# Kernel optimization log

Hardware: AMD Instinct MI355X
Metric: run time of the kernel (lower is better)

The kernel has to match this reference:

```python
import jax, jax.numpy as jnp
import numpy as np

N = 4096
IN_DIM = 256
OUT_DIM = 256
E = 131072


def setup_inputs() -> dict:
    key = jax.random.key(0)
    ks = jax.random.split(key, 8)
    x = jax.random.normal(ks[0], (N, IN_DIM), dtype=jnp.float32)
    edge_index = jax.random.randint(ks[1], (2, E), 0, N, dtype=jnp.int64)
    lap = jax.random.normal(ks[2], (N, N), dtype=jnp.float32)
    d_inv = jax.random.normal(ks[3], (N, N), dtype=jnp.float32)
    # parameters
    W_high = jax.random.normal(ks[4], (IN_DIM, OUT_DIM), dtype=jnp.float32) / np.sqrt(IN_DIM)
    W_conv = jax.random.normal(ks[5], (IN_DIM, OUT_DIM), dtype=jnp.float32) / np.sqrt(IN_DIM)
    b_conv = jnp.zeros((OUT_DIM,), dtype=jnp.float32)
    aL = jax.random.uniform(ks[6], (1,), dtype=jnp.float32)
    aH = jax.random.uniform(ks[7], (1,), dtype=jnp.float32)
    return {"x": x, "edge_index": edge_index, "lap": lap, "d_inv": d_inv,
            "W_high": W_high, "W_conv": W_conv, "b_conv": b_conv,
            "aL": aL, "aH": aH}


def _gcn_conv(x, edge_index, W, b, num_nodes):
    # PyG GCNConv: add self-loops, symmetric normalization, aggregate at target.
    src, dst = edge_index[0], edge_index[1]
    loop = jnp.arange(num_nodes, dtype=edge_index.dtype)
    src_f = jnp.concatenate([src, loop])
    dst_f = jnp.concatenate([dst, loop])
    deg = jax.ops.segment_sum(jnp.ones_like(dst_f, dtype=x.dtype), dst_f,
                              num_segments=num_nodes)
    deg_inv_sqrt = jnp.where(deg > 0, jax.lax.rsqrt(jnp.maximum(deg, 1e-12)), 0.0)
    norm = deg_inv_sqrt[src_f] * deg_inv_sqrt[dst_f]  # [E+N]
    xw = x @ W                                        # [N, out]
    msgs = xw[src_f] * norm[:, None]                  # [E+N, out]
    out = jax.ops.segment_sum(msgs, dst_f, num_segments=num_nodes)
    return out + b


def reference(x, edge_index, lap, d_inv, W_high, W_conv, b_conv, aL, aH):
    # high-pass branch: Lhp = d_inv @ lap @ d_inv; Hh = Lhp @ relu(x @ W_high)
    Lhp = (d_inv @ lap) @ d_inv
    Hh = Lhp @ jax.nn.relu(x @ W_high)
    # low-pass branch: GCNConv
    Hl = _gcn_conv(x, edge_index, W_conv, b_conv, x.shape[0])
    return aL * Hl + aH * Hh
```

## Files before the change

### kernel.cpp

```cpp
#include <hip/hip_runtime.h>

#define NN 4096
#define DD 256
#define EE 131072

typedef __attribute__((ext_vector_type(8))) short s16x8;
typedef __attribute__((ext_vector_type(4))) float f32x4;

__device__ __forceinline__ unsigned short f2bf(float f) {
  unsigned u = __builtin_bit_cast(unsigned, f);
  u += 0x7FFFu + ((u >> 16) & 1u);
  return (unsigned short)(u >> 16);
}

__device__ __forceinline__ ushort4 cvt4(f32x4 v) {
  ushort4 r;
  r.x = f2bf(v[0]); r.y = f2bf(v[1]); r.z = f2bf(v[2]); r.w = f2bf(v[3]);
  return r;
}

__device__ __forceinline__ unsigned cvt2_rhu(float a, float b) {
  unsigned ua = __builtin_bit_cast(unsigned, a) + 0x8000u;
  unsigned ub = __builtin_bit_cast(unsigned, b) + 0x8000u;
  return __builtin_amdgcn_perm(ub, ua, 0x07060302u);
}

__device__ __forceinline__ uint4 pack8(f32x4 a, f32x4 b) {
  uint4 r;
  r.x = cvt2_rhu(a[0], a[1]); r.y = cvt2_rhu(a[2], a[3]);
  r.z = cvt2_rhu(b[0], b[1]); r.w = cvt2_rhu(b[2], b[3]);
  return r;
}


__global__ void k_prep(const int* __restrict__ ei, int* __restrict__ deg,
                       const float* __restrict__ Wh, const float* __restrict__ Wc,
                       unsigned short* __restrict__ WFh, unsigned short* __restrict__ WFc) {
  int t = blockIdx.x * 256 + threadIdx.x;
  if (t < EE) {
    atomicAdd(&deg[ei[EE + t]], 1);
  } else {
    int idx = t - EE;
    int which = idx >> 16;
    int r = idx & 65535;
    int n = r & 255, k = r >> 8;
    const float* W = which ? Wc : Wh;
    unsigned short* WF = which ? WFc : WFh;
    long fidx = ((long)((n >> 4) * 8 + (k >> 5))) * 512 +
                (((k >> 3) & 3) * 16 + (n & 15)) * 8 + (k & 7);
    WF[fidx] = f2bf(W[k * 256 + n]);
  }
}

__global__ void k_scan(const int* __restrict__ deg, int* __restrict__ row_start,
                       float* __restrict__ dis) {
  __shared__ int part[1024];
  int t = threadIdx.x;
  int d0 = deg[4 * t + 0], d1 = deg[4 * t + 1], d2 = deg[4 * t + 2], d3 = deg[4 * t + 3];
  int s = d0 + d1 + d2 + d3;
  part[t] = s;
  __syncthreads();
  for (int off = 1; off < 1024; off <<= 1) {
    int add = (t >= off) ? part[t - off] : 0;
    __syncthreads();
    part[t] += add;
    __syncthreads();
  }
  int base = part[t] - s;
  row_start[4 * t + 0] = base;
  row_start[4 * t + 1] = base + d0;
  row_start[4 * t + 2] = base + d0 + d1;
  row_start[4 * t + 3] = base + d0 + d1 + d2;
  if (t == 1023) row_start[4096] = part[t];
  dis[4 * t + 0] = rsqrtf((float)d0 + 1.0f);
  dis[4 * t + 1] = rsqrtf((float)d1 + 1.0f);
  dis[4 * t + 2] = rsqrtf((float)d2 + 1.0f);
  dis[4 * t + 3] = rsqrtf((float)d3 + 1.0f);
}

__global__ void k_scatter(const int* __restrict__ ei, const int* __restrict__ row_start,
                          int* __restrict__ cursor, int* __restrict__ csr) {
  int e = blockIdx.x * 256 + threadIdx.x;
  if (e < EE) {
    int s = ei[e];
    int d = ei[EE + e];
    int p = atomicAdd(&cursor[d], 1);
    csr[row_start[d] + p] = s;
  }
}

__global__ __launch_bounds__(512) void k_xw(const float* __restrict__ x,
                                            const unsigned short* __restrict__ WFh,
                                            const unsigned short* __restrict__ WFc,
                                            unsigned short* __restrict__ RF,
                                            float* __restrict__ XWs,
                                            const float* __restrict__ dis) {
  __shared__ alignas(16) unsigned short Abuf[16][264];
  const int tid = threadIdx.x;
  const int w = tid >> 6, lane = tid & 63;
  const int quad = lane >> 4, l16 = lane & 15, quad8 = quad * 8;
  const int m0 = blockIdx.x * 16;

  {
    int srow = tid >> 5, scolf = (tid & 31) * 8;
    const float* ap = x + (long)(m0 + srow) * DD + scolf;
    f32x4 a0 = *(const f32x4*)ap;
    f32x4 a1 = *(const f32x4*)(ap + 4);
    *(uint4*)&Abuf[srow][scolf] = pack8(a0, a1);
  }
  __syncthreads();

  const bool hi = (w < 4);
  const int wo = hi ? w : (w - 4);
  const unsigned short* WF = hi ? WFh : WFc;
  const unsigned short* bp = WF + lane * 8;

  f32x4 acc[4] = {{0,0,0,0},{0,0,0,0},{0,0,0,0},{0,0,0,0}};
#pragma unroll
  for (int q = 0; q < 8; ++q) {
    s16x8 af = *(const s16x8*)&Abuf[l16][q * 32 + quad8];
#pragma unroll
    for (int s = 0; s < 4; ++s) {
      s16x8 bf = *(const s16x8*)(bp + ((long)((4 * wo + s) * 8 + q)) * 512);
      acc[s] = __builtin_amdgcn_mfma_f32_16x16x32_bf16(af, bf, acc[s], 0, 0, 0);
    }
  }

  if (hi) {
    const int kc = m0 >> 5;
    const int qp = ((m0 >> 4) & 1) * 2 + (quad >> 1);
    const int j0 = (quad & 1) * 4;
#pragma unroll
    for (int s = 0; s < 4; ++s) {
      int t = 4 * wo + s;
      f32x4 v = acc[s];
      f32x4 z;
      z[0] = v[0] > 0.f ? v[0] : 0.f;
      z[1] = v[1] > 0.f ? v[1] : 0.f;
      z[2] = v[2] > 0.f ? v[2] : 0.f;
      z[3] = v[3] > 0.f ? v[3] : 0.f;
      long idx = ((long)(t * 128 + kc)) * 512 + (qp * 16 + l16) * 8 + j0;
      *(ushort4*)(RF + idx) = cvt4(z);
    }
  } else {
    float dm[4];
#pragma unroll
    for (int r = 0; r < 4; ++r) dm[r] = dis[m0 + quad * 4 + r];
#pragma unroll
    for (int s = 0; s < 4; ++s) {
      int col = 64 * wo + 16 * s + l16;
#pragma unroll
      for (int r = 0; r < 4; ++r)
        XWs[(long)(m0 + quad * 4 + r) * DD + col] = dm[r] * acc[s][r];
    }
  }
}

__global__ void k_agg(const float* __restrict__ XWs, const int* __restrict__ row_start,
                      const int* __restrict__ csr, const float* __restrict__ dis,
                      float* __restrict__ Hl) {
  const int i = blockIdx.x;
  const int t = threadIdx.x;
  const int b0 = row_start[i], b1 = row_start[i + 1];
  float acc = XWs[(long)i * DD + t];
  int j = b0;
  for (; j + 4 <= b1; j += 4) {
    int s0 = csr[j], s1 = csr[j + 1], s2 = csr[j + 2], s3 = csr[j + 3];
    float v0 = XWs[(long)s0 * DD + t];
    float v1 = XWs[(long)s1 * DD + t];
    float v2 = XWs[(long)s2 * DD + t];
    float v3 = XWs[(long)s3 * DD + t];
    acc += (v0 + v1) + (v2 + v3);
  }
  for (; j < b1; ++j) acc += XWs[(long)csr[j] * DD + t];
  Hl[(long)i * DD + t] = dis[i] * acc;
}

template <int EPI>
__global__ __launch_bounds__(512) void k_mm2(const float* __restrict__ A,
                                             const unsigned short* __restrict__ BF,
                                             unsigned short* __restrict__ CF,
                                             float* __restrict__ outF,
                                             const float* __restrict__ Hl,
                                             const float* __restrict__ bconv,
                                             const float* __restrict__ aLp,
                                             const float* __restrict__ aHp) {
  __shared__ alignas(16) unsigned short Abuf[2][16][264];
  const int tid = threadIdx.x;
  const int w = tid >> 6, lane = tid & 63;
  const int quad = lane >> 4, l16 = lane & 15, quad8 = quad * 8;
  const int tile = blockIdx.x & 255, half = blockIdx.x >> 8;
  const int m0 = tile * 16;
  const int tglob = half * 8 + w;

  const int arow = tid >> 5;
  const int acolf = (tid & 31) * 8;
  const float* aptr = A + (long)(m0 + arow) * NN + acolf;

  {
    f32x4 c0 = *(const f32x4*)(aptr + 0);
    f32x4 c1 = *(const f32x4*)(aptr + 4);
    *(uint4*)&Abuf[0][arow][acolf] = pack8(c0, c1);
  }
  f32x4 anext[2];
  anext[0] = *(const f32x4*)(aptr + 256);
  anext[1] = *(const f32x4*)(aptr + 260);
  __syncthreads();

  f32x4 acc = {0, 0, 0, 0};
  const unsigned short* bbase = BF + ((long)tglob * 128) * 512 + lane * 8;

  for (int s = 0; s < 16; ++s) {
    const int cur = s & 1;
    f32x4 afut[2];
    if (s + 2 < 16) {
      afut[0] = *(const f32x4*)(aptr + (s + 2) * 256);
      afut[1] = *(const f32x4*)(aptr + (s + 2) * 256 + 4);
    } else {
      afut[0] = anext[0];
      afut[1] = anext[1];
    }

    const unsigned short* bs = bbase + ((long)s * 8) * 512;
#pragma unroll
    for (int q = 0; q < 8; ++q) {
      s16x8 bf = *(const s16x8*)(bs + q * 512);
      s16x8 af = *(const s16x8*)&Abuf[cur][l16][q * 32 + quad8];
      acc = __builtin_amdgcn_mfma_f32_16x16x32_bf16(af, bf, acc, 0, 0, 0);
    }

    if (s + 1 < 16) {
      *(uint4*)&Abuf[1 - cur][arow][acolf] = pack8(anext[0], anext[1]);
    }
    __syncthreads();
    anext[0] = afut[0];
    anext[1] = afut[1];
  }

  if constexpr (EPI == 0) {
    const int kc = tile >> 1;
    const int qp = (tile & 1) * 2 + (quad >> 1);
    const int j0 = (quad & 1) * 4;
    long idx = ((long)(tglob * 128 + kc)) * 512 + (qp * 16 + l16) * 8 + j0;
    *(ushort4*)(CF + idx) = cvt4(acc);
  } else {
    float(*obuf)[132] = reinterpret_cast<float(*)[132]>(&Abuf[0][0][0]);
#pragma unroll
    for (int r = 0; r < 4; ++r)
      obuf[quad * 4 + r][w * 16 + l16] = acc[r];
    __syncthreads();
    const float aLv = aLp[0], aHv = aHp[0];
    const int orow = tid >> 5;
    const int ocol = (tid & 31) * 4;
    const int gcol = half * 128 + ocol;
    f32x4 cc = *(const f32x4*)&obuf[orow][ocol];
    f32x4 h = *(const f32x4*)(Hl + (long)(m0 + orow) * DD + gcol);
    f32x4 bc = *(const f32x4*)(bconv + gcol);
    f32x4 res;
    res[0] = aHv * cc[0] + aLv * (h[0] + bc[0]);
    res[1] = aHv * cc[1] + aLv * (h[1] + bc[1]);
    res[2] = aHv * cc[2] + aLv * (h[2] + bc[2]);
    res[3] = aHv * cc[3] + aLv * (h[3] + bc[3]);
    *(f32x4*)(outF + (long)(m0 + orow) * DD + gcol) = res;
  }
}

extern "C" void kernel_launch(void* const* d_in, const int* in_sizes, int n_in,
                              void* d_out, int out_size, void* d_ws, size_t ws_size,
                              hipStream_t stream) {
  const float* x     = (const float*)d_in[0];
  const int*   ei    = (const int*)d_in[1];
  const float* lap   = (const float*)d_in[2];
  const float* dinv  = (const float*)d_in[3];
  const float* Wh    = (const float*)d_in[4];
  const float* Wc    = (const float*)d_in[5];
  const float* bconv = (const float*)d_in[6];
  const float* aL    = (const float*)d_in[7];
  const float* aH    = (const float*)d_in[8];
  float* out = (float*)d_out;
  char* ws = (char*)d_ws;

  int* deg        = (int*)(ws);
  int* cursor     = (int*)(ws + (16 << 10));
  int* row_start  = (int*)(ws + (32 << 10));
  int* csr        = (int*)(ws + (64 << 10));
  float* dis      = (float*)(ws + (576 << 10));
  unsigned short* WFh = (unsigned short*)(ws + (1l << 20));
  unsigned short* WFc = (unsigned short*)(ws + (1l << 20) + (128 << 10));
  unsigned short* RF  = (unsigned short*)(ws + (2l << 20));
  unsigned short* T1F = (unsigned short*)(ws + (4l << 20));
  unsigned short* T2F = (unsigned short*)(ws + (6l << 20));
  float* XWs = (float*)(ws + (8l << 20));
  float* Hl  = (float*)(ws + (12l << 20));

  hipMemsetAsync(ws, 0, 32 << 10, stream);

  k_prep<<<1024, 256, 0, stream>>>(ei, deg, Wh, Wc, WFh, WFc);
  k_scan<<<1, 1024, 0, stream>>>(deg, row_start, dis);
  k_scatter<<<512, 256, 0, stream>>>(ei, row_start, cursor, csr);
  k_xw<<<256, 512, 0, stream>>>(x, WFh, WFc, RF, XWs, dis);
  k_agg<<<4096, 256, 0, stream>>>(XWs, row_start, csr, dis, Hl);

  k_mm2<0><<<512, 512, 0, stream>>>(dinv, RF, T1F, nullptr, nullptr, nullptr, nullptr, nullptr);
  k_mm2<0><<<512, 512, 0, stream>>>(lap, T1F, T2F, nullptr, nullptr, nullptr, nullptr, nullptr);
  k_mm2<3><<<512, 512, 0, stream>>>(dinv, T2F, nullptr, out, Hl, bconv, aL, aH);
}
```

Before: 280.6 us.

## Restructure dense matmul to register-direct loads with 32x32 wave tiles

```diff
diff --git a/kernel.cpp b/kernel.cpp
--- a/kernel.cpp
+++ b/kernel.cpp
@@ -30,6 +30,11 @@
   r.x = cvt2_rhu(a[0], a[1]); r.y = cvt2_rhu(a[2], a[3]);
   r.z = cvt2_rhu(b[0], b[1]); r.w = cvt2_rhu(b[2], b[3]);
   return r;
+}
+
+__device__ __forceinline__ s16x8 pack8f(f32x4 a, f32x4 b) {
+  uint4 p = pack8(a, b);
+  return __builtin_bit_cast(s16x8, p);
 }
 
 
@@ -185,83 +190,82 @@
                                              const float* __restrict__ bconv,
                                              const float* __restrict__ aLp,
                                              const float* __restrict__ aHp) {
-  __shared__ alignas(16) unsigned short Abuf[2][16][264];
   const int tid = threadIdx.x;
   const int w = tid >> 6, lane = tid & 63;
-  const int quad = lane >> 4, l16 = lane & 15, quad8 = quad * 8;
-  const int tile = blockIdx.x & 255, half = blockIdx.x >> 8;
-  const int m0 = tile * 16;
-  const int tglob = half * 8 + w;
-
-  const int arow = tid >> 5;
-  const int acolf = (tid & 31) * 8;
-  const float* aptr = A + (long)(m0 + arow) * NN + acolf;
-
-  {
-    f32x4 c0 = *(const f32x4*)(aptr + 0);
-    f32x4 c1 = *(const f32x4*)(aptr + 4);
-    *(uint4*)&Abuf[0][arow][acolf] = pack8(c0, c1);
-  }
-  f32x4 anext[2];
-  anext[0] = *(const f32x4*)(aptr + 256);
-  anext[1] = *(const f32x4*)(aptr + 260);
-  __syncthreads();
-
-  f32x4 acc = {0, 0, 0, 0};
-  const unsigned short* bbase = BF + ((long)tglob * 128) * 512 + lane * 8;
-
-  for (int s = 0; s < 16; ++s) {
-    const int cur = s & 1;
-    f32x4 afut[2];
-    if (s + 2 < 16) {
-      afut[0] = *(const f32x4*)(aptr + (s + 2) * 256);
-      afut[1] = *(const f32x4*)(aptr + (s + 2) * 256 + 4);
-    } else {
-      afut[0] = anext[0];
-      afut[1] = anext[1];
+  const int quad = lane >> 4, l16 = lane & 15;
+  const int mblk = blockIdx.x & 127, nhalf = blockIdx.x >> 7;
+  const int msub = w & 1, nsub = w >> 1;
+  const int mrow = mblk * 32 + msub * 16 + l16;
+  const int t0 = nhalf * 8 + nsub * 2;
+
+  const float* ap = A + (long)mrow * NN + quad * 8;
+  const unsigned short* bp0 = BF + ((long)t0 * 128) * 512 + lane * 8;
+  const unsigned short* bp1 = bp0 + 128l * 512;
+
+  f32x4 xa0[4], xa1[4]; s16x8 xb0[4], xb1[4];
+  f32x4 ya0[4], ya1[4]; s16x8 yb0[4], yb1[4];
+  f32x4 acc0 = {0, 0, 0, 0}, acc1 = {0, 0, 0, 0};
+
+  const float* apx = ap;
+  const float* apy = ap + 128;
+  const unsigned short* b0x = bp0;
+  const unsigned short* b0y = bp0 + 4 * 512;
+  const unsigned short* b1x = bp1;
+  const unsigned short* b1y = bp1 + 4 * 512;
+
+#define LDG(a0v, a1v, b0v, b1v, apv, b0pv, b1pv)                 \
+  {                                                              \
+    _Pragma("unroll") for (int c = 0; c < 4; ++c) {              \
+      a0v[c] = *(const f32x4*)(apv + c * 32);                    \
+      a1v[c] = *(const f32x4*)(apv + c * 32 + 4);                \
+      b0v[c] = *(const s16x8*)(b0pv + c * 512);                  \
+      b1v[c] = *(const s16x8*)(b1pv + c * 512);                  \
+    }                                                            \
+    apv += 256; b0pv += 4096; b1pv += 4096;                      \
+  }
+
+#define CMP(a0v, a1v, b0v, b1v)                                              \
+  {                                                                          \
+    _Pragma("unroll") for (int c = 0; c < 4; ++c) {                          \
+      s16x8 af = pack8f(a0v[c], a1v[c]);                                     \
+      acc0 = __builtin_amdgcn_mfma_f32_16x16x32_bf16(af, b0v[c], acc0, 0, 0, 0); \
+      acc1 = __builtin_amdgcn_mfma_f32_16x16x32_bf16(af, b1v[c], acc1, 0, 0, 0); \
+    }                                                                        \
+  }
+
+  LDG(xa0, xa1, xb0, xb1, apx, b0x, b1x);
+  LDG(ya0, ya1, yb0, yb1, apy, b0y, b1y);
+
+#pragma unroll 1
+  for (int g = 0; g < 32; g += 2) {
+    CMP(xa0, xa1, xb0, xb1);
+    if (g + 2 < 32) LDG(xa0, xa1, xb0, xb1, apx, b0x, b1x);
+    CMP(ya0, ya1, yb0, yb1);
+    if (g + 3 < 32) LDG(ya0, ya1, yb0, yb1, apy, b0y, b1y);
+  }
+#undef LDG
+#undef CMP
+
+  if constexpr (EPI == 0) {
+    const int qp = msub * 2 + (quad >> 1);
+    const int j0 = (quad & 1) * 4;
+    long i0 = ((long)(t0 * 128 + mblk)) * 512 + (qp * 16 + l16) * 8 + j0;
+    long i1 = ((long)((t0 + 1) * 128 + mblk)) * 512 + (qp * 16 + l16) * 8 + j0;
+    *(ushort4*)(CF + i0) = cvt4(acc0);
+    *(ushort4*)(CF + i1) = cvt4(acc1);
+  } else {
+    const float aLv = aLp[0], aHv = aHp[0];
+    const int mr = mblk * 32 + msub * 16 + quad * 4;
+    const int c0 = t0 * 16 + l16;
+    const int c1 = c0 + 16;
+#pragma unroll
+    for (int r = 0; r < 4; ++r) {
+      int row = mr + r;
+      outF[(long)row * DD + c0] =
+          aHv * acc0[r] + aLv * (Hl[(long)row * DD + c0] + bconv[c0]);
+      outF[(long)row * DD + c1] =
+          aHv * acc1[r] + aLv * (Hl[(long)row * DD + c1] + bconv[c1]);
     }
-
-    const unsigned short* bs = bbase + ((long)s * 8) * 512;
-#pragma unroll
-    for (int q = 0; q < 8; ++q) {
-      s16x8 bf = *(const s16x8*)(bs + q * 512);
-      s16x8 af = *(const s16x8*)&Abuf[cur][l16][q * 32 + quad8];
-      acc = __builtin_amdgcn_mfma_f32_16x16x32_bf16(af, bf, acc, 0, 0, 0);
-    }
-
-    if (s + 1 < 16) {
-      *(uint4*)&Abuf[1 - cur][arow][acolf] = pack8(anext[0], anext[1]);
-    }
-    __syncthreads();
-    anext[0] = afut[0];
-    anext[1] = afut[1];
-  }
-
-  if constexpr (EPI == 0) {
-    const int kc = tile >> 1;
-    const int qp = (tile & 1) * 2 + (quad >> 1);
-    const int j0 = (quad & 1) * 4;
-    long idx = ((long)(tglob * 128 + kc)) * 512 + (qp * 16 + l16) * 8 + j0;
-    *(ushort4*)(CF + idx) = cvt4(acc);
-  } else {
-    float(*obuf)[132] = reinterpret_cast<float(*)[132]>(&Abuf[0][0][0]);
-#pragma unroll
-    for (int r = 0; r < 4; ++r)
-      obuf[quad * 4 + r][w * 16 + l16] = acc[r];
-    __syncthreads();
-    const float aLv = aLp[0], aHv = aHp[0];
-    const int orow = tid >> 5;
-    const int ocol = (tid & 31) * 4;
-    const int gcol = half * 128 + ocol;
-    f32x4 cc = *(const f32x4*)&obuf[orow][ocol];
-    f32x4 h = *(const f32x4*)(Hl + (long)(m0 + orow) * DD + gcol);
-    f32x4 bc = *(const f32x4*)(bconv + gcol);
-    f32x4 res;
-    res[0] = aHv * cc[0] + aLv * (h[0] + bc[0]);
-    res[1] = aHv * cc[1] + aLv * (h[1] + bc[1]);
-    res[2] = aHv * cc[2] + aLv * (h[2] + bc[2]);
-    res[3] = aHv * cc[3] + aLv * (h[3] + bc[3]);
-    *(f32x4*)(outF + (long)(m0 + orow) * DD + gcol) = res;
   }
 }
 
@@ -301,7 +305,7 @@
   k_xw<<<256, 512, 0, stream>>>(x, WFh, WFc, RF, XWs, dis);
   k_agg<<<4096, 256, 0, stream>>>(XWs, row_start, csr, dis, Hl);
 
-  k_mm2<0><<<512, 512, 0, stream>>>(dinv, RF, T1F, nullptr, nullptr, nullptr, nullptr, nullptr);
-  k_mm2<0><<<512, 512, 0, stream>>>(lap, T1F, T2F, nullptr, nullptr, nullptr, nullptr, nullptr);
-  k_mm2<3><<<512, 512, 0, stream>>>(dinv, T2F, nullptr, out, Hl, bconv, aL, aH);
-}
+  k_mm2<0><<<256, 512, 0, stream>>>(dinv, RF, T1F, nullptr, nullptr, nullptr, nullptr, nullptr);
+  k_mm2<0><<<256, 512, 0, stream>>>(lap, T1F, T2F, nullptr, nullptr, nullptr, nullptr, nullptr);
+  k_mm2<3><<<256, 512, 0, stream>>>(dinv, T2F, nullptr, out, Hl, bconv, aL, aH);
+}
```

Result: slower. 407.2 us (+45.1%).
